# Performance work log

Hardware: AMD Instinct MI355X
Metric: run time of the kernel (lower is better)

The kernel has to match this reference:

```python
import jax, jax.numpy as jnp
import numpy as np


def setup_inputs() -> dict:
    key = jax.random.key(0)
    ks = jax.random.split(key, 16)
    B, S, D = 2, 2048, 1024
    H, SH, RH = 16, 1, 3
    hd = D // H
    w = 1.0 / np.sqrt(D)
    return {
        "x": jax.random.normal(ks[0], (B, S, D), jnp.float32),
        "Wq": jax.random.normal(ks[1], (D, D), jnp.float32) * w,
        "bq": jnp.zeros((D,), jnp.float32),
        "Wk": jax.random.normal(ks[2], (D, D), jnp.float32) * w,
        "bk": jnp.zeros((D,), jnp.float32),
        "Wv": jax.random.normal(ks[3], (D, D), jnp.float32) * w,
        "bv": jnp.zeros((D,), jnp.float32),
        "Wproj": jax.random.normal(ks[4], (D, D), jnp.float32) * w,
        "bproj": jnp.zeros((D,), jnp.float32),
        "Wr": jax.random.normal(ks[5], (D, H - SH), jnp.float32) * w,
        "br": jnp.zeros((H - SH,), jnp.float32),
        "Ws": jax.random.normal(ks[6], (D, 2), jnp.float32) * w,
        "bs": jnp.zeros((2,), jnp.float32),
        "temperature": jnp.zeros((H, 1, 1), jnp.float32),
        "query_embedding": jax.random.truncated_normal(ks[7], -2.0, 2.0, (H, 1, hd), jnp.float32) * 0.02,
        "num_heads": H,
        "shared_heads": SH,
        "routed_heads": RH,
    }


def reference(x, Wq, bq, Wk, bk, Wv, bv, Wproj, bproj, Wr, br, Ws, bs,
              temperature, query_embedding, num_heads, shared_heads, routed_heads):
    B, S, D = x.shape
    H = num_heads
    hd = D // H

    def split_heads(t):  # [B,S,D] -> [B,H,S,hd]
        return t.reshape(B, S, H, hd).transpose(0, 2, 1, 3)

    q = split_heads(x @ Wq + bq)
    k = split_heads(x @ Wk + bk)
    v = split_heads(x @ Wv + bv)

    # L2-normalize q along head_dim, add learned query embedding, scale by softplus(temperature)
    q_norm = q * jax.lax.rsqrt(jnp.sum(q * q, axis=-1, keepdims=True) + 1e-12)
    q_scaled = (q_norm + query_embedding[None]) * jax.nn.softplus(temperature)[None]

    attn = jnp.einsum('bhqd,bhkd->bhqk', q_scaled, k) / jnp.sqrt(jnp.float32(hd))
    attn = jax.nn.softmax(attn, axis=-1)
    o = jnp.einsum('bhqk,bhkd->bhqd', attn, v)
    o = o.transpose(0, 2, 1, 3).reshape(B, S, D)  # [B,S,D]

    # Routed-head gating via top-k router
    gates = jax.nn.softmax(o @ Wr + br, axis=-1)          # [B,S,H-SH]
    _, idx = jax.lax.top_k(gates, routed_heads)           # [B,S,RH]
    mask = jax.nn.one_hot(idx, H - shared_heads, dtype=gates.dtype).sum(axis=2)
    routed_gates = gates * mask * jnp.float32(routed_heads)

    # Shared-head gating
    sw = jax.nn.softmax(o @ Ws + bs, axis=-1)             # [B,S,2]
    shared_gates = sw * jnp.float32(shared_heads)
    w0 = sw * 2.0
    shared_gates = w0[..., 0:1] * shared_gates
    routed_gates = w0[..., 1:2] * routed_gates
    masked_gates = jnp.concatenate([shared_gates, routed_gates], axis=-1)

    # einsum('bnh,bnd->bnd') sums over h: scales o by sum of gates
    o = masked_gates.sum(axis=-1, keepdims=True) * o
    return o @ Wproj + bproj
```

## Files before the change

### kernel.cpp

```cpp
#include <hip/hip_runtime.h>
#include <hip/hip_bf16.h>

typedef unsigned short ushort_t;
typedef unsigned int uint_t;

typedef __attribute__((ext_vector_type(8))) short bf8;
typedef __attribute__((ext_vector_type(4))) float f4;
typedef __attribute__((ext_vector_type(16))) float f16v;

__device__ __forceinline__ float bf2f(ushort_t u) {
    unsigned int x = ((unsigned int)u) << 16;
    return __uint_as_float(x);
}
__device__ __forceinline__ ushort_t f2bf(float f) {
    unsigned int x = __float_as_uint(f);
    unsigned int r = x + 0x7fffu + ((x >> 16) & 1u);
    return (ushort_t)(r >> 16);
}
__device__ __forceinline__ uint_t pack2bf(float a, float b) {
    return (uint_t)f2bf(a) | ((uint_t)f2bf(b) << 16);
}
__device__ __forceinline__ uint_t pack2bf_fast(float a, float b) {
    uint_t au = __float_as_uint(a) + 0x8000u;
    uint_t bu = __float_as_uint(b) + 0x8000u;
    return __builtin_amdgcn_perm(bu, au, 0x07060302);
}
__device__ __forceinline__ float exp2_fast(float x) {
    float r; asm("v_exp_f32 %0, %1" : "=v"(r) : "v"(x)); return r;
}
__device__ __forceinline__ uint_t cvtpk_bf16(float lo, float hi) {
    uint_t r; asm("v_cvt_pk_bf16_f32 %0, %1, %2" : "=v"(r) : "v"(lo), "v"(hi)); return r;
}
__device__ __forceinline__ void pl32swap(uint_t &a, uint_t &b) {
    asm("v_permlane32_swap_b32 %0, %1" : "+v"(a), "+v"(b));
}

__device__ __forceinline__ void gl2lds16(const ushort_t* g, ushort_t* l) {
    __builtin_amdgcn_global_load_lds(
        (const __attribute__((address_space(1))) void*)g,
        (__attribute__((address_space(3))) void*)l, 16, 0, 0);
}

__device__ __forceinline__ void waitl0() {
    asm volatile("s_waitcnt lgkmcnt(0)" ::: "memory");
    __builtin_amdgcn_sched_barrier(0);
}

__global__ __launch_bounds__(256)
void prep(const float* __restrict__ x, ushort_t* __restrict__ xb,
          const float* __restrict__ Wr, const float* __restrict__ Ws,
          ushort_t* __restrict__ Wg,
          const float* __restrict__ W0, const float* __restrict__ W1,
          const float* __restrict__ W2, const float* __restrict__ W3,
          ushort_t* __restrict__ T0, ushort_t* __restrict__ T1,
          ushort_t* __restrict__ T2, ushort_t* __restrict__ T3)
{
    __shared__ float tile[32][33];
    int bid = blockIdx.x;
    int t = threadIdx.x;
    if (bid < 4096) {
        int i = bid * 256 + t;
        float4 v = ((const float4*)x)[i];
        uint2 o;
        o.x = pack2bf(v.x, v.y);
        o.y = pack2bf(v.z, v.w);
        ((uint2*)xb)[i] = o;
    } else if (bid < 4224) {
        int idx = (bid - 4096) * 256 + t;
        int c = idx >> 10, d = idx & 1023;
        float v = 0.f;
        if (c < 15) v = Wr[(size_t)d * 15 + c];
        else if (c < 17) v = Ws[(size_t)d * 2 + (c - 15)];
        Wg[idx] = f2bf(v);
    } else {
        int idx = bid - 4224;
        int z = idx >> 10, r10 = idx & 1023;
        int k0 = (r10 & 31) * 32, n0 = (r10 >> 5) * 32;
        const float* W; ushort_t* T;
        switch (z) {
            case 0: W = W0; T = T0; break;
            case 1: W = W1; T = T1; break;
            case 2: W = W2; T = T2; break;
            default: W = W3; T = T3; break;
        }
        int r = t >> 3, c4 = (t & 7) * 4;
        float4 v = *(const float4*)&W[(size_t)(k0 + r) * 1024 + n0 + c4];
        tile[r][c4 + 0] = v.x; tile[r][c4 + 1] = v.y;
        tile[r][c4 + 2] = v.z; tile[r][c4 + 3] = v.w;
        __syncthreads();
        int n = t >> 3, kk = (t & 7) * 4;
        uint2 o;
        o.x = pack2bf(tile[kk][n], tile[kk + 1][n]);
        o.y = pack2bf(tile[kk + 2][n], tile[kk + 3][n]);
        *(uint2*)&T[(size_t)(n0 + n) * 1024 + k0 + kk] = o;
    }
}

__global__ __launch_bounds__(256)
void gemmQKV(const ushort_t* __restrict__ A, const ushort_t* __restrict__ Wt3,
             const float* __restrict__ bq, const float* __restrict__ bk,
             const float* __restrict__ bv,
             ushort_t* __restrict__ Qb, ushort_t* __restrict__ Kw,
             ushort_t* __restrict__ VTw,
             const float* __restrict__ temp, const float* __restrict__ emb)
{
    const int K = 1024;
    __shared__ ushort_t As[128 * 64];
    __shared__ ushort_t Bs[128 * 64];

    int t = threadIdx.x;
    int m0 = blockIdx.x * 128;
    int y = blockIdx.y;
    int region = y >> 3;
    int n0 = (y & 7) * 128;

    int lane = t & 63, w = t >> 6;
    int lm = lane & 15, quad = lane >> 4;
    int wm = (w >> 1) * 64, wn = (w & 1) * 64;

    f4 acc[4][4] = {};

    int srow = t >> 3;
    int schunk = ((t & 7) ^ (srow & 7)) * 8;
    const ushort_t* pA = &A[(size_t)(m0 + srow) * K + schunk];
    const ushort_t* pB = &Wt3[(size_t)(y * 128 + srow) * K + schunk];
    const size_t rstep = (size_t)32 * K;

    for (int k0 = 0; k0 < K; k0 += 64) {
        #pragma unroll
        for (int j = 0; j < 4; j++) {
            gl2lds16(pA + j * rstep, &As[(t + j * 256) * 8]);
            gl2lds16(pB + j * rstep, &Bs[(t + j * 256) * 8]);
        }
        pA += 64; pB += 64;
        __syncthreads();

        #pragma unroll
        for (int ks = 0; ks < 2; ks++) {
            int rc = ((ks * 4 + quad) ^ (lm & 7)) * 8;
            bf8 af[4], bfr[4];
            #pragma unroll
            for (int mi = 0; mi < 4; mi++)
                af[mi] = *(bf8*)&As[(wm + mi * 16 + lm) * 64 + rc];
            #pragma unroll
            for (int ni = 0; ni < 4; ni++)
                bfr[ni] = *(bf8*)&Bs[(wn + ni * 16 + lm) * 64 + rc];
            if (region == 2) {
                #pragma unroll
                for (int mi = 0; mi < 4; mi++)
                #pragma unroll
                for (int ni = 0; ni < 4; ni++)
                    acc[mi][ni] = __builtin_amdgcn_mfma_f32_16x16x32_bf16(af[mi], bfr[ni], acc[mi][ni], 0, 0, 0);
            } else {
                #pragma unroll
                for (int ni = 0; ni < 4; ni++)
                #pragma unroll
                for (int mi = 0; mi < 4; mi++)
                    acc[ni][mi] = __builtin_amdgcn_mfma_f32_16x16x32_bf16(bfr[ni], af[mi], acc[ni][mi], 0, 0, 0);
            }
        }
        __syncthreads();
    }

    if (region == 0) {
        int head = (n0 + wn) >> 6;
        float sp = log1pf(__expf(temp[head]));
        float qs = sp * 0.18033688011112042f;
        f4 bv4[4], ev4[4];
        #pragma unroll
        for (int ni = 0; ni < 4; ni++) {
            bv4[ni] = *(const f4*)&bq[n0 + wn + ni * 16 + quad * 4];
            ev4[ni] = *(const f4*)&emb[head * 64 + ni * 16 + quad * 4];
        }
        #pragma unroll
        for (int mi = 0; mi < 4; mi++) {
            float v[4][4];
            float ss = 0.f;
            #pragma unroll
            for (int ni = 0; ni < 4; ni++)
            #pragma unroll
            for (int i = 0; i < 4; i++) {
                v[ni][i] = acc[ni][mi][i] + bv4[ni][i];
                ss += v[ni][i] * v[ni][i];
            }
            ss += __shfl_xor(ss, 16, 64);
            ss += __shfl_xor(ss, 32, 64);
            float rs = rsqrtf(ss + 1e-12f);
            int tok = m0 + wm + mi * 16 + lm;
            int b = tok >> 11, s = tok & 2047;
            size_t rowb = (((size_t)(b * 16 + head)) * 2048 + s) * 64;
            #pragma unroll
            for (int ni = 0; ni < 4; ni++) {
                uint2 o;
                o.x = pack2bf((v[ni][0] * rs + ev4[ni][0]) * qs,
                              (v[ni][1] * rs + ev4[ni][1]) * qs);
                o.y = pack2bf((v[ni][2] * rs + ev4[ni][2]) * qs,
                              (v[ni][3] * rs + ev4[ni][3]) * qs);
                *(uint2*)&Qb[rowb + ni * 16 + quad * 4] = o;
            }
        }
    } else if (region == 1) {
        int head = (n0 + wn) >> 6;
        f4 bv4[4];
        #pragma unroll
        for (int ni = 0; ni < 4; ni++)
            bv4[ni] = *(const f4*)&bk[n0 + wn + ni * 16 + quad * 4];
        #pragma unroll
        for (int mi = 0; mi < 4; mi++) {
            int tok = m0 + wm + mi * 16 + lm;
            int b = tok >> 11, s = tok & 2047;
            size_t rowb = (((size_t)(b * 16 + head)) * 2048 + s) * 64;
            #pragma unroll
            for (int ni = 0; ni < 4; ni++) {
                uint2 o;
                o.x = pack2bf(acc[ni][mi][0] + bv4[ni][0], acc[ni][mi][1] + bv4[ni][1]);
                o.y = pack2bf(acc[ni][mi][2] + bv4[ni][2], acc[ni][mi][3] + bv4[ni][3]);
                *(uint2*)&Kw[rowb + ni * 16 + quad * 4] = o;
            }
        }
    } else {
        float bvv[4];
        #pragma unroll
        for (int ni = 0; ni < 4; ni++) bvv[ni] = bv[n0 + wn + ni * 16 + lm];
        #pragma unroll
        for (int mi = 0; mi < 4; mi++) {
            int gr0 = m0 + wm + mi * 16 + quad * 4;
            int b = gr0 >> 11, s0 = gr0 & 2047;
            #pragma unroll
            for (int ni = 0; ni < 4; ni++) {
                int gc = n0 + wn + ni * 16 + lm;
                int h = gc >> 6, d = gc & 63;
                uint2 o;
                o.x = pack2bf(acc[mi][ni][0] + bvv[ni], acc[mi][ni][1] + bvv[ni]);
                o.y = pack2bf(acc[mi][ni][2] + bvv[ni], acc[mi][ni][3] + bvv[ni]);
                *(uint2*)&VTw[(((size_t)(b * 16 + h)) * 64 + d) * 2048 + s0] = o;
            }
        }
    }
}

__global__ __launch_bounds__(256)
void gemmP(const ushort_t* __restrict__ A, const ushort_t* __restrict__ Wt,
           const float* __restrict__ bias, const float* __restrict__ G,
           float* __restrict__ out, int M, int N, int K)
{
    __shared__ ushort_t As[128 * 64];
    __shared__ ushort_t Bs[128 * 64];

    int t = threadIdx.x;
    int m0 = blockIdx.x * 128, n0 = blockIdx.y * 128;
    int lane = t & 63, w = t >> 6;
    int lm = lane & 15, quad = lane >> 4;
    int wm = (w >> 1) * 64, wn = (w & 1) * 64;

    f4 acc[4][4] = {};

    int srow = t >> 3;
    int schunk = ((t & 7) ^ (srow & 7)) * 8;
    const ushort_t* pA = &A[(size_t)(m0 + srow) * K + schunk];
    const ushort_t* pB = &Wt[(size_t)(n0 + srow) * K + schunk];
    const size_t rstep = (size_t)32 * K;

    for (int k0 = 0; k0 < K; k0 += 64) {
        #pragma unroll
        for (int j = 0; j < 4; j++) {
            gl2lds16(pA + j * rstep, &As[(t + j * 256) * 8]);
            gl2lds16(pB + j * rstep, &Bs[(t + j * 256) * 8]);
        }
        pA += 64; pB += 64;
        __syncthreads();

        #pragma unroll
        for (int ks = 0; ks < 2; ks++) {
            int rc = ((ks * 4 + quad) ^ (lm & 7)) * 8;
            bf8 af[4], bfr[4];
            #pragma unroll
            for (int mi = 0; mi < 4; mi++)
                af[mi] = *(bf8*)&As[(wm + mi * 16 + lm) * 64 + rc];
            #pragma unroll
            for (int ni = 0; ni < 4; ni++)
                bfr[ni] = *(bf8*)&Bs[(wn + ni * 16 + lm) * 64 + rc];
            #pragma unroll
            for (int ni = 0; ni < 4; ni++)
            #pragma unroll
            for (int mi = 0; mi < 4; mi++)
                acc[ni][mi] = __builtin_amdgcn_mfma_f32_16x16x32_bf16(bfr[ni], af[mi], acc[ni][mi], 0, 0, 0);
        }
        __syncthreads();
    }

    f4 bv4[4];
    #pragma unroll
    for (int ni = 0; ni < 4; ni++)
        bv4[ni] = *(const f4*)&bias[n0 + wn + ni * 16 + quad * 4];
    #pragma unroll
    for (int mi = 0; mi < 4; mi++) {
        int tok = m0 + wm + mi * 16 + lm;
        float g = G[tok];
        size_t rowb = (size_t)tok * N + n0 + wn;
        #pragma unroll
        for (int ni = 0; ni < 4; ni++) {
            f4 o;
            #pragma unroll
            for (int i = 0; i < 4; i++) o[i] = g * acc[ni][mi][i] + bv4[ni][i];
            *(f4*)&out[rowb + ni * 16 + quad * 4] = o;
        }
    }
}

__global__ __launch_bounds__(256)
void attn(const ushort_t* __restrict__ Q, const ushort_t* __restrict__ K,
          const ushort_t* __restrict__ VT, ushort_t* __restrict__ Opart,
          float* __restrict__ Lw)
{
    __shared__ ushort_t Ks[64 * 72];
    __shared__ ushort_t Vt[64 * 72];

    int t = threadIdx.x, lane = t & 63, w = t >> 6;
    int l31 = lane & 31;
    uint_t hi = lane >> 5;
    int bid = blockIdx.x;
    int bh = bid & 31, qt = (bid >> 5) & 15, ks = bid >> 9;
    size_t base = (size_t)bh * 2048 * 64;

    int tok = qt * 128 + w * 32 + l31;
    const ushort_t* qp = &Q[base + (size_t)tok * 64 + hi * 8];
    bf8 qa[4];
    #pragma unroll
    for (int c = 0; c < 4; c++) qa[c] = *(const bf8*)(qp + c * 16);

    float l_part = 0.f;
    f16v o_acc[2] = {};

    int sr = t >> 3, sc = (t & 7) * 8;
    const ushort_t* kp = &K[base + (size_t)(ks * 1024 + sr) * 64 + sc];
    const ushort_t* vp = &VT[base + (size_t)sr * 2048 + ks * 1024 + sc];

    uint4 rk0 = *(const uint4*)(kp);
    uint4 rk1 = *(const uint4*)(kp + 32 * 64);
    uint4 rv0 = *(const uint4*)(vp);
    uint4 rv1 = *(const uint4*)(vp + 32 * 2048);
    kp += 64 * 64; vp += 64;

    for (int it = 0; it < 16; ++it) {
        *(uint4*)&Ks[sr * 72 + sc] = rk0;
        *(uint4*)&Ks[(sr + 32) * 72 + sc] = rk1;
        *(uint4*)&Vt[sr * 72 + sc] = rv0;
        *(uint4*)&Vt[(sr + 32) * 72 + sc] = rv1;
        __syncthreads();

        rk0 = *(const uint4*)(kp);
        rk1 = *(const uint4*)(kp + 32 * 64);
        rv0 = *(const uint4*)(vp);
        rv1 = *(const uint4*)(vp + 32 * 2048);
        kp += 64 * 64; vp += 64;

        bf8 pf[4];
        #pragma unroll
        for (int kt2 = 0; kt2 < 2; kt2++) {
            f16v s = {};
            #pragma unroll
            for (int c = 0; c < 4; c++) {
                bf8 kf = *(bf8*)&Ks[(kt2 * 32 + l31) * 72 + c * 16 + hi * 8];
                s = __builtin_amdgcn_mfma_f32_32x32x16_bf16(kf, qa[c], s, 0, 0, 0);
            }
            uint_t px[4], py[4];
            #pragma unroll
            for (int g = 0; g < 4; g++) {
                float p0 = exp2_fast(s[g * 4 + 0]);
                float p1 = exp2_fast(s[g * 4 + 1]);
                float p2 = exp2_fast(s[g * 4 + 2]);
                float p3 = exp2_fast(s[g * 4 + 3]);
                l_part += (p0 + p1) + (p2 + p3);
                px[g] = cvtpk_bf16(p0, p1);
                py[g] = cvtpk_bf16(p2, p3);
            }
            #pragma unroll
            for (int cc = 0; cc < 2; cc++) {
                uint_t ax = px[2 * cc], bx = px[2 * cc + 1];
                uint_t ay = py[2 * cc], by = py[2 * cc + 1];
                pl32swap(ax, bx);
                pl32swap(ay, by);
                uint4 u;
                u.x = ax; u.y = ay; u.z = bx; u.w = by;
                pf[kt2 * 2 + cc] = *(bf8*)&u;
            }
        }

        #pragma unroll
        for (int c = 0; c < 4; c++) {
            #pragma unroll
            for (int dt = 0; dt < 2; dt++) {
                bf8 vf = *(bf8*)&Vt[(dt * 32 + l31) * 72 + c * 16 + hi * 8];
                o_acc[dt] = __builtin_amdgcn_mfma_f32_32x32x16_bf16(vf, pf[c], o_acc[dt], 0, 0, 0);
            }
        }
        __syncthreads();
    }

    l_part += __shfl_xor(l_part, 32, 64);
    if (hi == 0) Lw[((size_t)ks * 32 + bh) * 2048 + tok] = l_part;

    size_t pbase = (((size_t)(ks * 32 + bh)) * 2048 + tok) * 64;
    #pragma unroll
    for (int dt = 0; dt < 2; dt++)
    #pragma unroll
    for (int g = 0; g < 4; g++) {
        int d0 = dt * 32 + g * 8 + hi * 4;
        uint2 o;
        o.x = pack2bf_fast(o_acc[dt][g * 4 + 0], o_acc[dt][g * 4 + 1]);
        o.y = pack2bf_fast(o_acc[dt][g * 4 + 2], o_acc[dt][g * 4 + 3]);
        *(uint2*)&Opart[pbase + d0] = o;
    }
}

__global__ __launch_bounds__(256)
void fuseCR(const ushort_t* __restrict__ Opart, const float* __restrict__ Lw,
            const ushort_t* __restrict__ Wg, const float* __restrict__ br,
            const float* __restrict__ bs, ushort_t* __restrict__ Ob,
            float* __restrict__ G)
{
    __shared__ ushort_t Obs[16 * 1032];
    __shared__ float rl_s[16][16];
    __shared__ float Ls[16][21];

    int t = threadIdx.x;
    int tokg0 = blockIdx.x * 16;
    int b = tokg0 >> 11, st0 = tokg0 & 2047;

    {
        int h = t >> 4, tt = t & 15;
        size_t row = (size_t)(b * 16 + h) * 2048 + st0 + tt;
        rl_s[h][tt] = 1.f / (Lw[row] + Lw[65536 + row]);
    }
    __syncthreads();

    {
        int tt = t >> 4, dc = (t & 15) * 4;
        #pragma unroll 4
        for (int h = 0; h < 16; h++) {
            size_t rbase = ((size_t)(b * 16 + h) * 2048 + st0 + tt) * 64 + dc;
            uint2 p0 = *(const uint2*)&Opart[rbase];
            uint2 p1 = *(const uint2*)&Opart[4194304 + rbase];
            float rl = rl_s[h][tt];
            float v0 = (bf2f(p0.x & 0xffff) + bf2f(p1.x & 0xffff)) * rl;
            float v1 = (bf2f(p0.x >> 16)   + bf2f(p1.x >> 16))   * rl;
            float v2 = (bf2f(p0.y & 0xffff) + bf2f(p1.y & 0xffff)) * rl;
            float v3 = (bf2f(p0.y >> 16)   + bf2f(p1.y >> 16))   * rl;
            uint2 o;
            o.x = pack2bf(v0, v1);
            o.y = pack2bf(v2, v3);
            *(uint2*)&Obs[tt * 1032 + h * 64 + dc] = o;
            *(uint2*)&Ob[((size_t)(tokg0 + tt)) * 1024 + h * 64 + dc] = o;
        }
    }
    __syncthreads();

    if (t < 64) {
        int lm = t & 15, quad = t >> 4;
        const ushort_t* b0p = &Wg[(size_t)lm * 1024 + quad * 8];
        const ushort_t* b1p = &Wg[(size_t)(16 + lm) * 1024 + quad * 8];
        f4 acc0 = {}, acc1 = {};
        for (int k0 = 0; k0 < 1024; k0 += 32) {
            bf8 a  = *(const bf8*)&Obs[lm * 1032 + k0 + quad * 8];
            bf8 b0 = *(const bf8*)(b0p + k0);
            bf8 b1 = *(const bf8*)(b1p + k0);
            acc0 = __builtin_amdgcn_mfma_f32_16x16x32_bf16(a, b0, acc0, 0, 0, 0);
            acc1 = __builtin_amdgcn_mfma_f32_16x16x32_bf16(a, b1, acc1, 0, 0, 0);
        }
        #pragma unroll
        for (int i = 0; i < 4; i++) {
            int tl = quad * 4 + i;
            Ls[tl][lm] = acc0[i];
            if (lm == 0) Ls[tl][16] = acc1[i];
        }
        waitl0();

        if (t < 16) {
            float v[15];
            float mx = -1e30f;
            #pragma unroll
            for (int c = 0; c < 15; c++) { v[c] = Ls[t][c] + br[c]; mx = fmaxf(mx, v[c]); }
            float sum = 0.f;
            #pragma unroll
            for (int c = 0; c < 15; c++) { v[c] = __expf(v[c] - mx); sum += v[c]; }
            float inv = 1.f / sum;
            float t3 = 0.f;
            for (int r = 0; r < 3; r++) {
                int bi = 0; float bv = -1e30f;
                #pragma unroll
                for (int c = 0; c < 15; c++) if (v[c] > bv) { bv = v[c]; bi = c; }
                t3 += bv; v[bi] = -1e30f;
            }
            t3 *= inv;
            float a0 = Ls[t][15] + bs[0], a1 = Ls[t][16] + bs[1];
            float m2 = fmaxf(a0, a1);
            float e0 = __expf(a0 - m2), e1 = __expf(a1 - m2);
            G[tokg0 + t] = (2.f * e0 + 6.f * e1 * t3) / (e0 + e1);
        }
    }
}

extern "C" void kernel_launch(void* const* d_in, const int* in_sizes, int n_in,
                              void* d_out, int out_size, void* d_ws, size_t ws_size,
                              hipStream_t stream)
{
    const float* x     = (const float*)d_in[0];
    const float* Wq    = (const float*)d_in[1];
    const float* bq    = (const float*)d_in[2];
    const float* Wk    = (const float*)d_in[3];
    const float* bk    = (const float*)d_in[4];
    const float* Wv    = (const float*)d_in[5];
    const float* bv    = (const float*)d_in[6];
    const float* Wproj = (const float*)d_in[7];
    const float* bproj = (const float*)d_in[8];
    const float* Wr    = (const float*)d_in[9];
    const float* br    = (const float*)d_in[10];
    const float* Ws    = (const float*)d_in[11];
    const float* bs    = (const float*)d_in[12];
    const float* temp  = (const float*)d_in[13];
    const float* emb   = (const float*)d_in[14];

    const int M = 4096, N = 1024, Kd = 1024;

    char* ws = (char*)d_ws;
    ushort_t* Kw    = (ushort_t*)ws;
    ushort_t* VTw   = (ushort_t*)(ws + 8388608);
    ushort_t* Qb    = (ushort_t*)(ws + 16777216);
    ushort_t* Wtp   = (ushort_t*)(ws + 25165824);
    float*    Gw    = (float*)(ws + 27262976);
    ushort_t* Wg    = (ushort_t*)(ws + 27279360);
    float*    Lw    = (float*)(ws + 27344896);
    ushort_t* Wt3   = (ushort_t*)(ws + 27869184);
    ushort_t* xb    = (ushort_t*)(ws + 34160640);
    ushort_t* Opart = (ushort_t*)(ws + 27869184);
    ushort_t* Ob    = Qb;

    prep<<<8320, 256, 0, stream>>>(x, xb, Wr, Ws, Wg, Wq, Wk, Wv, Wproj,
        Wt3, Wt3 + 1048576, Wt3 + 2097152, Wtp);

    gemmQKV<<<dim3(32, 24), 256, 0, stream>>>(xb, Wt3, bq, bk, bv,
        Qb, Kw, VTw, temp, emb);

    attn<<<1024, 256, 0, stream>>>(Qb, Kw, VTw, Opart, Lw);

    fuseCR<<<256, 256, 0, stream>>>(Opart, Lw, Wg, br, bs, Ob, Gw);

    gemmP<<<dim3(32, 8), 256, 0, stream>>>(Ob, Wtp, bproj, Gw, (float*)d_out, M, N, Kd);
}
```

Measured before the change: 242.6 us.

## Enlarge QKV GEMM tiles to 256x256 with double-buffered LDS prefetch

```diff
diff --git a/kernel.cpp b/kernel.cpp
--- a/kernel.cpp
+++ b/kernel.cpp
@@ -96,7 +96,7 @@
     }
 }
 
-__global__ __launch_bounds__(256)
+__global__ __launch_bounds__(512, 2)
 void gemmQKV(const ushort_t* __restrict__ A, const ushort_t* __restrict__ Wt3,
              const float* __restrict__ bq, const float* __restrict__ bk,
              const float* __restrict__ bv,
@@ -105,82 +105,107 @@
              const float* __restrict__ temp, const float* __restrict__ emb)
 {
     const int K = 1024;
-    __shared__ ushort_t As[128 * 64];
-    __shared__ ushort_t Bs[128 * 64];
+    const int NT = 16;
+    __shared__ ushort_t As[2][256 * 64];
+    __shared__ ushort_t Bs[2][256 * 64];
 
     int t = threadIdx.x;
-    int m0 = blockIdx.x * 128;
-    int y = blockIdx.y;
-    int region = y >> 3;
-    int n0 = (y & 7) * 128;
+    int m0 = blockIdx.x * 256;
+    int yt = blockIdx.y;
+    int region = yt >> 2;
+    int n0r = (yt & 3) * 256;
+    int n0g = yt * 256;
 
     int lane = t & 63, w = t >> 6;
     int lm = lane & 15, quad = lane >> 4;
-    int wm = (w >> 1) * 64, wn = (w & 1) * 64;
-
-    f4 acc[4][4] = {};
+    int wr = w >> 2, wc = w & 3;
+    int wm = wr * 128, wn = wc * 64;
+
+    f4 acc[32] = {};
 
     int srow = t >> 3;
     int schunk = ((t & 7) ^ (srow & 7)) * 8;
-    const ushort_t* pA = &A[(size_t)(m0 + srow) * K + schunk];
-    const ushort_t* pB = &Wt3[(size_t)(y * 128 + srow) * K + schunk];
-    const size_t rstep = (size_t)32 * K;
-
-    for (int k0 = 0; k0 < K; k0 += 64) {
+    const ushort_t* pA0 = &A[(size_t)(m0 + srow) * K + schunk];
+    const ushort_t* pB0 = &Wt3[(size_t)(n0g + srow) * K + schunk];
+    const size_t rstep = (size_t)64 * K;
+
+    {
         #pragma unroll
         for (int j = 0; j < 4; j++) {
-            gl2lds16(pA + j * rstep, &As[(t + j * 256) * 8]);
-            gl2lds16(pB + j * rstep, &Bs[(t + j * 256) * 8]);
-        }
-        pA += 64; pB += 64;
-        __syncthreads();
+            gl2lds16(pA0 + j * rstep, &As[0][(t + j * 512) * 8]);
+            gl2lds16(pB0 + j * rstep, &Bs[0][(t + j * 512) * 8]);
+        }
+    }
+    asm volatile("s_waitcnt vmcnt(0)" ::: "memory");
+    __builtin_amdgcn_sched_barrier(0);
+    __builtin_amdgcn_s_barrier();
+
+    int cur = 0;
+    #pragma clang loop unroll(disable)
+    for (int kt = 0; kt < NT; ++kt) {
+        if (kt + 1 < NT) {
+            const ushort_t* sA = pA0 + (kt + 1) * 64;
+            const ushort_t* sB = pB0 + (kt + 1) * 64;
+            int nb = cur ^ 1;
+            #pragma unroll
+            for (int j = 0; j < 4; j++) {
+                gl2lds16(sA + j * rstep, &As[nb][(t + j * 512) * 8]);
+                gl2lds16(sB + j * rstep, &Bs[nb][(t + j * 512) * 8]);
+            }
+        }
+        __builtin_amdgcn_sched_barrier(0);
 
         #pragma unroll
         for (int ks = 0; ks < 2; ks++) {
             int rc = ((ks * 4 + quad) ^ (lm & 7)) * 8;
-            bf8 af[4], bfr[4];
-            #pragma unroll
-            for (int mi = 0; mi < 4; mi++)
-                af[mi] = *(bf8*)&As[(wm + mi * 16 + lm) * 64 + rc];
+            bf8 af[8], bfr[4];
+            #pragma unroll
+            for (int mi = 0; mi < 8; mi++)
+                af[mi] = *(bf8*)&As[cur][(wm + mi * 16 + lm) * 64 + rc];
             #pragma unroll
             for (int ni = 0; ni < 4; ni++)
-                bfr[ni] = *(bf8*)&Bs[(wn + ni * 16 + lm) * 64 + rc];
+                bfr[ni] = *(bf8*)&Bs[cur][(wn + ni * 16 + lm) * 64 + rc];
+            __builtin_amdgcn_s_setprio(1);
             if (region == 2) {
                 #pragma unroll
-                for (int mi = 0; mi < 4; mi++)
+                for (int mi = 0; mi < 8; mi++)
                 #pragma unroll
                 for (int ni = 0; ni < 4; ni++)
-                    acc[mi][ni] = __builtin_amdgcn_mfma_f32_16x16x32_bf16(af[mi], bfr[ni], acc[mi][ni], 0, 0, 0);
+                    acc[mi * 4 + ni] = __builtin_amdgcn_mfma_f32_16x16x32_bf16(af[mi], bfr[ni], acc[mi * 4 + ni], 0, 0, 0);
             } else {
                 #pragma unroll
                 for (int ni = 0; ni < 4; ni++)
                 #pragma unroll
-                for (int mi = 0; mi < 4; mi++)
-                    acc[ni][mi] = __builtin_amdgcn_mfma_f32_16x16x32_bf16(bfr[ni], af[mi], acc[ni][mi], 0, 0, 0);
-            }
-        }
-        __syncthreads();
+                for (int mi = 0; mi < 8; mi++)
+                    acc[ni * 8 + mi] = __builtin_amdgcn_mfma_f32_16x16x32_bf16(bfr[ni], af[mi], acc[ni * 8 + mi], 0, 0, 0);
+            }
+            __builtin_amdgcn_s_setprio(0);
+        }
+        asm volatile("s_waitcnt vmcnt(0)" ::: "memory");
+        __builtin_amdgcn_sched_barrier(0);
+        __builtin_amdgcn_s_barrier();
+        cur ^= 1;
     }
 
     if (region == 0) {
-        int head = (n0 + wn) >> 6;
+        int head = (n0r + wn) >> 6;
         float sp = log1pf(__expf(temp[head]));
         float qs = sp * 0.18033688011112042f;
         f4 bv4[4], ev4[4];
         #pragma unroll
         for (int ni = 0; ni < 4; ni++) {
-            bv4[ni] = *(const f4*)&bq[n0 + wn + ni * 16 + quad * 4];
+            bv4[ni] = *(const f4*)&bq[n0r + wn + ni * 16 + quad * 4];
             ev4[ni] = *(const f4*)&emb[head * 64 + ni * 16 + quad * 4];
         }
         #pragma unroll
-        for (int mi = 0; mi < 4; mi++) {
+        for (int mi = 0; mi < 8; mi++) {
             float v[4][4];
             float ss = 0.f;
             #pragma unroll
             for (int ni = 0; ni < 4; ni++)
             #pragma unroll
             for (int i = 0; i < 4; i++) {
-                v[ni][i] = acc[ni][mi][i] + bv4[ni][i];
+                v[ni][i] = acc[ni * 8 + mi][i] + bv4[ni][i];
                 ss += v[ni][i] * v[ni][i];
             }
             ss += __shfl_xor(ss, 16, 64);
@@ -200,39 +225,39 @@
             }
         }
     } else if (region == 1) {
-        int head = (n0 + wn) >> 6;
+        int head = (n0r + wn) >> 6;
         f4 bv4[4];
         #pragma unroll
         for (int ni = 0; ni < 4; ni++)
-            bv4[ni] = *(const f4*)&bk[n0 + wn + ni * 16 + quad * 4];
-        #pragma unroll
-        for (int mi = 0; mi < 4; mi++) {
+            bv4[ni] = *(const f4*)&bk[n0r + wn + ni * 16 + quad * 4];
+        #pragma unroll
+        for (int mi = 0; mi < 8; mi++) {
             int tok = m0 + wm + mi * 16 + lm;
             int b = tok >> 11, s = tok & 2047;
             size_t rowb = (((size_t)(b * 16 + head)) * 2048 + s) * 64;
             #pragma unroll
             for (int ni = 0; ni < 4; ni++) {
                 uint2 o;
-                o.x = pack2bf(acc[ni][mi][0] + bv4[ni][0], acc[ni][mi][1] + bv4[ni][1]);
-                o.y = pack2bf(acc[ni][mi][2] + bv4[ni][2], acc[ni][mi][3] + bv4[ni][3]);
+                o.x = pack2bf(acc[ni * 8 + mi][0] + bv4[ni][0], acc[ni * 8 + mi][1] + bv4[ni][1]);
+                o.y = pack2bf(acc[ni * 8 + mi][2] + bv4[ni][2], acc[ni * 8 + mi][3] + bv4[ni][3]);
                 *(uint2*)&Kw[rowb + ni * 16 + quad * 4] = o;
             }
         }
     } else {
         float bvv[4];
         #pragma unroll
-        for (int ni = 0; ni < 4; ni++) bvv[ni] = bv[n0 + wn + ni * 16 + lm];
-        #pragma unroll
-        for (int mi = 0; mi < 4; mi++) {
+        for (int ni = 0; ni < 4; ni++) bvv[ni] = bv[n0r + wn + ni * 16 + lm];
+        #pragma unroll
+        for (int mi = 0; mi < 8; mi++) {
             int gr0 = m0 + wm + mi * 16 + quad * 4;
             int b = gr0 >> 11, s0 = gr0 & 2047;
             #pragma unroll
             for (int ni = 0; ni < 4; ni++) {
-                int gc = n0 + wn + ni * 16 + lm;
+                int gc = n0r + wn + ni * 16 + lm;
                 int h = gc >> 6, d = gc & 63;
                 uint2 o;
-                o.x = pack2bf(acc[mi][ni][0] + bvv[ni], acc[mi][ni][1] + bvv[ni]);
-                o.y = pack2bf(acc[mi][ni][2] + bvv[ni], acc[mi][ni][3] + bvv[ni]);
+                o.x = pack2bf(acc[mi * 4 + ni][0] + bvv[ni], acc[mi * 4 + ni][1] + bvv[ni]);
+                o.y = pack2bf(acc[mi * 4 + ni][2] + bvv[ni], acc[mi * 4 + ni][3] + bvv[ni]);
                 *(uint2*)&VTw[(((size_t)(b * 16 + h)) * 64 + d) * 2048 + s0] = o;
             }
         }
@@ -539,7 +564,7 @@
     prep<<<8320, 256, 0, stream>>>(x, xb, Wr, Ws, Wg, Wq, Wk, Wv, Wproj,
         Wt3, Wt3 + 1048576, Wt3 + 2097152, Wtp);
 
-    gemmQKV<<<dim3(32, 24), 256, 0, stream>>>(xb, Wt3, bq, bk, bv,
+    gemmQKV<<<dim3(16, 12), 512, 0, stream>>>(xb, Wt3, bq, bk, bv,
         Qb, Kw, VTw, temp, emb);
 
     attn<<<1024, 256, 0, stream>>>(Qb, Kw, VTw, Opart, Lw);
```

New measurement: 340.2 us. +40.2%, slower.
